# Kernel optimization log

Hardware: AMD Instinct MI355X
Metric: run time of the kernel (lower is better)

The kernel has to match this reference:

```python
import jax, jax.numpy as jnp
import numpy as np

N_NODES = 100000
N_EDGES = 1600000
D = 64


def setup_inputs() -> dict:
    key = jax.random.key(0)
    k1, k2, k3, k4 = jax.random.split(key, 4)
    graph_embedding = jax.random.normal(k1, (N_NODES, D), dtype=jnp.float32)
    # xavier_uniform_ on a (1, D) tensor: bound = sqrt(6 / (1 + D))
    bound = float(np.sqrt(6.0 / (1 + D)))
    weight = jax.random.uniform(k2, (1, D), dtype=jnp.float32, minval=-bound, maxval=bound)
    src = jax.random.randint(k3, (N_EDGES,), 0, N_NODES, dtype=jnp.int32)
    dst = jax.random.randint(k4, (N_EDGES,), 0, N_NODES, dtype=jnp.int32)
    return {"graph_embedding": graph_embedding, "weight": weight, "src": src, "dst": dst}


def reference(graph_embedding, weight, src, dst):
    # emb = elu(x * w) per node, then copy_u/sum over edges:
    # out[d] = sum over edges (s -> d) of emb[s]
    emb = jax.nn.elu(graph_embedding * weight)          # [N, D]
    msgs = emb[src]                                     # [E, D] gathered source messages
    out = jax.ops.segment_sum(msgs, dst, num_segments=graph_embedding.shape[0])
    return out
```

## Files before the change

kernel.cpp:

```cpp
#include <hip/hip_runtime.h>

#define D 64
#define D4 (D / 4)
#define SBSHIFT 9
#define SBROWS 512
#define CHUNK_E 8192
#define STAGE_CAP 8704
#define NCH_MAX 256
#define NSB_MAX 256

typedef float f32x4 __attribute__((ext_vector_type(4)));

__device__ __forceinline__ float elu1(float z) {
    return z > 0.0f ? z : expm1f(z);
}

__device__ __forceinline__ unsigned int bfpair(float a, float b) {
    unsigned int ua = __float_as_uint(a);
    unsigned int ub = __float_as_uint(b);
    ua = (ua + 0x7FFFu + ((ua >> 16) & 1u)) >> 16;
    ub = (ub + 0x7FFFu + ((ub >> 16) & 1u)) & 0xFFFF0000u;
    return ub | ua;
}

__device__ __forceinline__ float bl16(int u) {
    return __uint_as_float((unsigned)u << 16);
}
__device__ __forceinline__ float bh16(int u) {
    return __uint_as_float((unsigned)u & 0xFFFF0000u);
}

__global__ __launch_bounds__(512) void chunk_emb_kernel(
        const float* __restrict__ x, const float* __restrict__ w,
        uint4* __restrict__ emb16,
        const int* __restrict__ src, const int* __restrict__ dst,
        int* __restrict__ slots_lin,
        int* __restrict__ cbase,
        int total8, int n_edges) {
    __shared__ int hist[256], base[256], cur[256];
    __shared__ int wsum[4];
    __shared__ int stage[CHUNK_E];
    const int tid = threadIdx.x;
    const int lane = tid & 63, wid = tid >> 6;

    if (tid < 256) hist[tid] = 0;
    const int gsz = gridDim.x * 512;
    for (int i = blockIdx.x * 512 + tid; i < total8; i += gsz) {
        f32x4 a = __builtin_nontemporal_load((const f32x4*)x + 2 * i);
        f32x4 b = __builtin_nontemporal_load((const f32x4*)x + 2 * i + 1);
        float4 wa = ((const float4*)w)[(2 * i) & 15];
        float4 wb = ((const float4*)w)[(2 * i + 1) & 15];
        uint4 o;
        o.x = bfpair(elu1(a.x * wa.x), elu1(a.y * wa.y));
        o.y = bfpair(elu1(a.z * wa.z), elu1(a.w * wa.w));
        o.z = bfpair(elu1(b.x * wb.x), elu1(b.y * wb.y));
        o.w = bfpair(elu1(b.z * wb.z), elu1(b.w * wb.w));
        emb16[i] = o;
    }

    const int c0  = blockIdx.x * CHUNK_E;
    const int kn  = min(CHUNK_E, n_edges - c0);
    const int kn4 = kn >> 2;
    const int tail = kn & 3;
    __syncthreads();
    const int4* dst4 = (const int4*)(dst + c0);
    for (int k = tid; k < kn4; k += 512) {
        int4 dv = dst4[k];
        atomicAdd(&hist[dv.x >> SBSHIFT], 1);
        atomicAdd(&hist[dv.y >> SBSHIFT], 1);
        atomicAdd(&hist[dv.z >> SBSHIFT], 1);
        atomicAdd(&hist[dv.w >> SBSHIFT], 1);
    }
    if (tid < tail)
        atomicAdd(&hist[dst[c0 + (kn4 << 2) + tid] >> SBSHIFT], 1);
    __syncthreads();
    int h = 0, incl = 0;
    if (tid < 256) {
        h = hist[tid];
        incl = h;
        #pragma unroll
        for (int off = 1; off < 64; off <<= 1) {
            int t = __shfl_up(incl, off, 64);
            if (lane >= off) incl += t;
        }
        if (lane == 63) wsum[wid] = incl;
    }
    __syncthreads();
    if (tid < 256) {
        int pre = 0;
        for (int k = 0; k < wid; k++) pre += wsum[k];
        int e = pre + incl - h;
        base[tid] = e;
        cur[tid]  = e;
    }
    __syncthreads();
    const int4* src4 = (const int4*)(src + c0);
    for (int k = tid; k < kn4; k += 512) {
        int4 dv = dst4[k];
        int4 sv = src4[k];
        int pos;
        pos = atomicAdd(&cur[dv.x >> SBSHIFT], 1);
        stage[pos] = ((dv.x & (SBROWS - 1)) << 17) | sv.x;
        pos = atomicAdd(&cur[dv.y >> SBSHIFT], 1);
        stage[pos] = ((dv.y & (SBROWS - 1)) << 17) | sv.y;
        pos = atomicAdd(&cur[dv.z >> SBSHIFT], 1);
        stage[pos] = ((dv.z & (SBROWS - 1)) << 17) | sv.z;
        pos = atomicAdd(&cur[dv.w >> SBSHIFT], 1);
        stage[pos] = ((dv.w & (SBROWS - 1)) << 17) | sv.w;
    }
    if (tid < tail) {
        int k = (kn4 << 2) + tid;
        int d = dst[c0 + k], s = src[c0 + k];
        int pos = atomicAdd(&cur[d >> SBSHIFT], 1);
        stage[pos] = ((d & (SBROWS - 1)) << 17) | s;
    }
    __syncthreads();
    for (int j = tid; j < kn; j += 512)
        slots_lin[c0 + j] = stage[j];
    if (tid < 256) cbase[blockIdx.x * 257 + tid] = base[tid];
    if (tid == 0)  cbase[blockIdx.x * 257 + 256] = kn;
}

__global__ __launch_bounds__(512) void fine_sort_kernel(
        const int* __restrict__ slots_lin,
        const int* __restrict__ cbase,
        int* __restrict__ sorted2,
        int* __restrict__ node_off,
        int n_nodes, int NCH) {
    __shared__ int rstart[NCH_MAX], rc[NCH_MAX];
    __shared__ int counts[SBROWS], cur[SBROWS];
    __shared__ int wsum[8], swa[8], swt[8];
    __shared__ int stage_out[STAGE_CAP];
    const int s = blockIdx.x;
    const int tid = threadIdx.x;
    const int wid = tid >> 6, lane = tid & 63;
    const int sg = tid >> 4, l16 = tid & 15;

    int va = 0, vt = 0;
    if (tid < NCH) {
        int a = cbase[tid * 257 + s];
        int b = cbase[tid * 257 + s + 1];
        rstart[tid] = tid * CHUNK_E + a;
        rc[tid] = b - a;
        va = a;
        vt = b - a;
    }
    #pragma unroll
    for (int off = 1; off < 64; off <<= 1) {
        va += __shfl_xor(va, off, 64);
        vt += __shfl_xor(vt, off, 64);
    }
    if (lane == 0) { swa[wid] = va; swt[wid] = vt; }
    counts[tid] = 0;
    __syncthreads();
    int sbb = 0, T = 0;
    #pragma unroll
    for (int k = 0; k < 8; k++) { sbb += swa[k]; T += swt[k]; }
    const bool fast = (T <= STAGE_CAP);
    for (int c = sg; c < NCH; c += 32) {
        int n = rc[c], st = rstart[c];
        for (int j = l16; j < n; j += 16)
            atomicAdd(&counts[((unsigned)slots_lin[st + j]) >> 17], 1);
    }
    __syncthreads();
    int v = counts[tid];
    int incl = v;
    #pragma unroll
    for (int off = 1; off < 64; off <<= 1) {
        int t = __shfl_up(incl, off, 64);
        if (lane >= off) incl += t;
    }
    if (lane == 63) wsum[wid] = incl;
    __syncthreads();
    int pre = 0;
    for (int k = 0; k < wid; k++) pre += wsum[k];
    int e0 = pre + incl - v;
    cur[tid] = fast ? e0 : sbb + e0;
    int g0 = (s << SBSHIFT) + tid;
    if (g0 < n_nodes) node_off[g0] = sbb + e0;
    if (s == gridDim.x - 1 && tid == 0) node_off[n_nodes] = sbb + T;
    __syncthreads();
    for (int c = sg; c < NCH; c += 32) {
        int n = rc[c], st = rstart[c];
        for (int j = l16; j < n; j += 16) {
            int pl = slots_lin[st + j];
            int r = ((unsigned)pl) >> 17;
            int pos = atomicAdd(&cur[r], 1);
            if (fast) stage_out[pos] = pl & 0x1FFFF;
            else      sorted2[pos]   = pl & 0x1FFFF;
        }
    }
    __syncthreads();
    if (fast) {
        for (int i = tid; i < T; i += 512)
            sorted2[sbb + i] = stage_out[i];
    }
}

__global__ void gather_sum_kernel(const unsigned int* __restrict__ emb16,
                                  const int* __restrict__ sorted2,
                                  const int* __restrict__ node_off,
                                  float* __restrict__ out, int n_nodes) {
    int wave = (blockIdx.x * blockDim.x + threadIdx.x) >> 6;
    if (wave >= n_nodes) return;
    const int lane = threadIdx.x & 63;
    const int g = lane >> 3;
    const int c = lane & 7;
    const int beg = node_off[wave], end = node_off[wave + 1];
    const int deg = end - beg;
    const int dmain = min(deg, 64);
    const int4* row = (const int4*)emb16;

    int myidx = 0;
    if (lane < dmain) myidx = __builtin_nontemporal_load(sorted2 + beg + lane);

    float acc[8] = {0.f, 0.f, 0.f, 0.f, 0.f, 0.f, 0.f, 0.f};

    for (int base = 0; base < dmain; base += 32) {
        const int m = dmain - base;
        int s0 = __shfl(myidx, base + g, 64);
        int s1 = __shfl(myidx, base + g + 8, 64);
        int s2 = __shfl(myidx, base + g + 16, 64);
        int s3 = __shfl(myidx, base + g + 24, 64);
        int4 u0 = make_int4(0, 0, 0, 0);
        int4 u1 = make_int4(0, 0, 0, 0);
        int4 u2 = make_int4(0, 0, 0, 0);
        int4 u3 = make_int4(0, 0, 0, 0);
        if (g < m)      u0 = row[s0 * 8 + c];
        if (g + 8 < m)  u1 = row[s1 * 8 + c];
        if (g + 16 < m) u2 = row[s2 * 8 + c];
        if (g + 24 < m) u3 = row[s3 * 8 + c];
        acc[0] += bl16(u0.x) + bl16(u1.x) + bl16(u2.x) + bl16(u3.x);
        acc[1] += bh16(u0.x) + bh16(u1.x) + bh16(u2.x) + bh16(u3.x);
        acc[2] += bl16(u0.y) + bl16(u1.y) + bl16(u2.y) + bl16(u3.y);
        acc[3] += bh16(u0.y) + bh16(u1.y) + bh16(u2.y) + bh16(u3.y);
        acc[4] += bl16(u0.z) + bl16(u1.z) + bl16(u2.z) + bl16(u3.z);
        acc[5] += bh16(u0.z) + bh16(u1.z) + bh16(u2.z) + bh16(u3.z);
        acc[6] += bl16(u0.w) + bl16(u1.w) + bl16(u2.w) + bl16(u3.w);
        acc[7] += bh16(u0.w) + bh16(u1.w) + bh16(u2.w) + bh16(u3.w);
    }
    for (int e = beg + 64 + g; e < end; e += 8) {
        int s0 = __builtin_nontemporal_load(sorted2 + e);
        int4 u0 = row[s0 * 8 + c];
        acc[0] += bl16(u0.x); acc[1] += bh16(u0.x);
        acc[2] += bl16(u0.y); acc[3] += bh16(u0.y);
        acc[4] += bl16(u0.z); acc[5] += bh16(u0.z);
        acc[6] += bl16(u0.w); acc[7] += bh16(u0.w);
    }
    #pragma unroll
    for (int off = 8; off <= 32; off <<= 1) {
        #pragma unroll
        for (int k = 0; k < 8; k++) acc[k] += __shfl_xor(acc[k], off, 64);
    }
    if (g == 0) {
        f32x4* out4 = (f32x4*)out;
        f32x4 o0 = {acc[0], acc[1], acc[2], acc[3]};
        f32x4 o1 = {acc[4], acc[5], acc[6], acc[7]};
        __builtin_nontemporal_store(o0, out4 + wave * D4 + c * 2);
        __builtin_nontemporal_store(o1, out4 + wave * D4 + c * 2 + 1);
    }
}

__global__ void zero_out_kernel(float* __restrict__ out, int total4) {
    int i = blockIdx.x * blockDim.x + threadIdx.x;
    if (i < total4) ((float4*)out)[i] = make_float4(0.f, 0.f, 0.f, 0.f);
}

__global__ void scatter_fused_kernel(const float* __restrict__ x,
                                     const float* __restrict__ w,
                                     const int* __restrict__ src,
                                     const int* __restrict__ dst,
                                     float* __restrict__ out, int n_edges) {
    int t = blockIdx.x * blockDim.x + threadIdx.x;
    int e = t >> 4;
    int c = t & 15;
    if (e >= n_edges) return;
    int s = src[e];
    int d = dst[e];
    float4 xv = ((const float4*)x)[s * D4 + c];
    float4 wv = ((const float4*)w)[c];
    float* o = out + d * D + c * 4;
    unsafeAtomicAdd(o + 0, elu1(xv.x * wv.x));
    unsafeAtomicAdd(o + 1, elu1(xv.y * wv.y));
    unsafeAtomicAdd(o + 2, elu1(xv.z * wv.z));
    unsafeAtomicAdd(o + 3, elu1(xv.w * wv.w));
}

extern "C" void kernel_launch(void* const* d_in, const int* in_sizes, int n_in,
                              void* d_out, int out_size, void* d_ws, size_t ws_size,
                              hipStream_t stream) {
    const float* x   = (const float*)d_in[0];
    const float* w   = (const float*)d_in[1];
    const int*   src = (const int*)d_in[2];
    const int*   dst = (const int*)d_in[3];
    float* out = (float*)d_out;

    const int n_nodes = in_sizes[0] / D;
    const int n_edges = in_sizes[2];
    const int total4  = n_nodes * D4;
    const int total8  = n_nodes * 8;
    const int block = 256;

    const int NSB = (n_nodes + SBROWS - 1) >> SBSHIFT;
    const int NCH = (n_edges + CHUNK_E - 1) / CHUNK_E;

    auto align16 = [](size_t v) { return (v + 15) & ~size_t(15); };
    const size_t emb_b      = align16((size_t)n_nodes * D * 2);
    const size_t slots_b    = align16((size_t)NCH * CHUNK_E * 4);
    const size_t cbase_b    = align16((size_t)NCH * 257 * 4);
    const size_t sorted2_b  = align16((size_t)n_edges * 4);
    const size_t nodeoff_b  = align16((size_t)(n_nodes + 1) * 4);
    const size_t need = emb_b + slots_b + cbase_b + sorted2_b + nodeoff_b;

    if (ws_size >= need && n_nodes <= 131072 && NSB <= NSB_MAX && NCH <= NCH_MAX) {
        char* p = (char*)d_ws;
        unsigned int* emb16 = (unsigned int*)p;  p += emb_b;
        int* slots_lin = (int*)p;  p += slots_b;
        int* cbase     = (int*)p;  p += cbase_b;
        int* sorted2   = (int*)p;  p += sorted2_b;
        int* node_off  = (int*)p;

        chunk_emb_kernel<<<NCH, 512, 0, stream>>>(
            x, w, (uint4*)emb16, src, dst, slots_lin, cbase, total8, n_edges);
        fine_sort_kernel<<<NSB, 512, 0, stream>>>(
            slots_lin, cbase, sorted2, node_off, n_nodes, NCH);
        const int wave_blocks = (n_nodes * 64 + block - 1) / block;
        gather_sum_kernel<<<wave_blocks, block, 0, stream>>>(
            emb16, sorted2, node_off, out, n_nodes);
    } else {
        zero_out_kernel<<<(total4 + block - 1) / block, block, 0, stream>>>(out, total4);
        const int nt = n_edges * 16;
        scatter_fused_kernel<<<(nt + block - 1) / block, block, 0, stream>>>(
            x, w, src, dst, out, n_edges);
    }
}
```

Baseline: 149.7 us.

## Gather eight nodes per wavefront and halve sort chunk and superblock sizes

The gather kernel now assigns eight destination nodes to each wavefront, one per 8-lane group, instead of one node per wave. The wave preloads up to 192 neighbour indices into registers, picks them by shuffle, and drops the cross-group reduction. This removes the idle lanes that low-degree nodes (average degree 16) leave in a 64-lane wave. The sort now uses 4096-edge chunks and 256-row superblocks, so there are twice as many blocks per kernel and the histogram arrays are indexed by NSB. The cost is load imbalance inside a wave, since every group loops to the largest degree among its eight nodes.

New measurement: 141.0 us. -5.8%, faster.

```diff
diff --git a/kernel.cpp b/kernel.cpp
--- a/kernel.cpp
+++ b/kernel.cpp
@@ -2,12 +2,12 @@
 
 #define D 64
 #define D4 (D / 4)
-#define SBSHIFT 9
-#define SBROWS 512
-#define CHUNK_E 8192
-#define STAGE_CAP 8704
-#define NCH_MAX 256
-#define NSB_MAX 256
+#define SBSHIFT 8
+#define SBROWS 256
+#define CHUNK_E 4096
+#define STAGE_CAP 4608
+#define NCH_MAX 512
+#define NSB_MAX 512
 
 typedef float f32x4 __attribute__((ext_vector_type(4)));
 
@@ -36,14 +36,14 @@
         const int* __restrict__ src, const int* __restrict__ dst,
         int* __restrict__ slots_lin,
         int* __restrict__ cbase,
-        int total8, int n_edges) {
-    __shared__ int hist[256], base[256], cur[256];
-    __shared__ int wsum[4];
+        int total8, int n_edges, int NSB) {
+    __shared__ int hist[NSB_MAX], base[NSB_MAX], cur[NSB_MAX];
+    __shared__ int wsum[8];
     __shared__ int stage[CHUNK_E];
     const int tid = threadIdx.x;
     const int lane = tid & 63, wid = tid >> 6;
 
-    if (tid < 256) hist[tid] = 0;
+    hist[tid] = 0;
     const int gsz = gridDim.x * 512;
     for (int i = blockIdx.x * 512 + tid; i < total8; i += gsz) {
         f32x4 a = __builtin_nontemporal_load((const f32x4*)x + 2 * i);
@@ -74,19 +74,16 @@
     if (tid < tail)
         atomicAdd(&hist[dst[c0 + (kn4 << 2) + tid] >> SBSHIFT], 1);
     __syncthreads();
-    int h = 0, incl = 0;
-    if (tid < 256) {
-        h = hist[tid];
-        incl = h;
-        #pragma unroll
-        for (int off = 1; off < 64; off <<= 1) {
-            int t = __shfl_up(incl, off, 64);
-            if (lane >= off) incl += t;
-        }
-        if (lane == 63) wsum[wid] = incl;
-    }
-    __syncthreads();
-    if (tid < 256) {
+    int h = hist[tid];
+    int incl = h;
+    #pragma unroll
+    for (int off = 1; off < 64; off <<= 1) {
+        int t = __shfl_up(incl, off, 64);
+        if (lane >= off) incl += t;
+    }
+    if (lane == 63) wsum[wid] = incl;
+    __syncthreads();
+    {
         int pre = 0;
         for (int k = 0; k < wid; k++) pre += wsum[k];
         int e = pre + incl - h;
@@ -117,8 +114,8 @@
     __syncthreads();
     for (int j = tid; j < kn; j += 512)
         slots_lin[c0 + j] = stage[j];
-    if (tid < 256) cbase[blockIdx.x * 257 + tid] = base[tid];
-    if (tid == 0)  cbase[blockIdx.x * 257 + 256] = kn;
+    if (tid < NSB) cbase[blockIdx.x * (NSB + 1) + tid] = base[tid];
+    if (tid == 0)  cbase[blockIdx.x * (NSB + 1) + NSB] = kn;
 }
 
 __global__ __launch_bounds__(512) void fine_sort_kernel(
@@ -126,10 +123,10 @@
         const int* __restrict__ cbase,
         int* __restrict__ sorted2,
         int* __restrict__ node_off,
-        int n_nodes, int NCH) {
+        int n_nodes, int NCH, int NSB) {
     __shared__ int rstart[NCH_MAX], rc[NCH_MAX];
     __shared__ int counts[SBROWS], cur[SBROWS];
-    __shared__ int wsum[8], swa[8], swt[8];
+    __shared__ int wsum[4], swa[8], swt[8];
     __shared__ int stage_out[STAGE_CAP];
     const int s = blockIdx.x;
     const int tid = threadIdx.x;
@@ -138,8 +135,8 @@
 
     int va = 0, vt = 0;
     if (tid < NCH) {
-        int a = cbase[tid * 257 + s];
-        int b = cbase[tid * 257 + s + 1];
+        int a = cbase[tid * (NSB + 1) + s];
+        int b = cbase[tid * (NSB + 1) + s + 1];
         rstart[tid] = tid * CHUNK_E + a;
         rc[tid] = b - a;
         va = a;
@@ -151,7 +148,7 @@
         vt += __shfl_xor(vt, off, 64);
     }
     if (lane == 0) { swa[wid] = va; swt[wid] = vt; }
-    counts[tid] = 0;
+    if (tid < SBROWS) counts[tid] = 0;
     __syncthreads();
     int sbb = 0, T = 0;
     #pragma unroll
@@ -163,21 +160,26 @@
             atomicAdd(&counts[((unsigned)slots_lin[st + j]) >> 17], 1);
     }
     __syncthreads();
-    int v = counts[tid];
-    int incl = v;
-    #pragma unroll
-    for (int off = 1; off < 64; off <<= 1) {
-        int t = __shfl_up(incl, off, 64);
-        if (lane >= off) incl += t;
-    }
-    if (lane == 63) wsum[wid] = incl;
-    __syncthreads();
-    int pre = 0;
-    for (int k = 0; k < wid; k++) pre += wsum[k];
-    int e0 = pre + incl - v;
-    cur[tid] = fast ? e0 : sbb + e0;
-    int g0 = (s << SBSHIFT) + tid;
-    if (g0 < n_nodes) node_off[g0] = sbb + e0;
+    int v = 0, incl = 0;
+    if (tid < SBROWS) {
+        v = counts[tid];
+        incl = v;
+        #pragma unroll
+        for (int off = 1; off < 64; off <<= 1) {
+            int t = __shfl_up(incl, off, 64);
+            if (lane >= off) incl += t;
+        }
+        if (lane == 63) wsum[wid] = incl;
+    }
+    __syncthreads();
+    if (tid < SBROWS) {
+        int pre = 0;
+        for (int k = 0; k < wid; k++) pre += wsum[k];
+        int e0 = pre + incl - v;
+        cur[tid] = fast ? e0 : sbb + e0;
+        int g0 = (s << SBSHIFT) + tid;
+        if (g0 < n_nodes) node_off[g0] = sbb + e0;
+    }
     if (s == gridDim.x - 1 && tid == 0) node_off[n_nodes] = sbb + T;
     __syncthreads();
     for (int c = sg; c < NCH; c += 32) {
@@ -197,39 +199,71 @@
     }
 }
 
+__device__ __forceinline__ int pick_idx(int p, int m0, int m1, int m2,
+                                        const int* __restrict__ s2, int W0) {
+    int a  = __shfl(m0, p & 63, 64);
+    int b  = __shfl(m1, p & 63, 64);
+    int cc = __shfl(m2, p & 63, 64);
+    int r = p < 64 ? a : (p < 128 ? b : cc);
+    if (p >= 192) r = s2[W0 + p];
+    return r;
+}
+
 __global__ void gather_sum_kernel(const unsigned int* __restrict__ emb16,
                                   const int* __restrict__ sorted2,
                                   const int* __restrict__ node_off,
                                   float* __restrict__ out, int n_nodes) {
-    int wave = (blockIdx.x * blockDim.x + threadIdx.x) >> 6;
-    if (wave >= n_nodes) return;
+    const int wv = (blockIdx.x * blockDim.x + threadIdx.x) >> 6;
     const int lane = threadIdx.x & 63;
     const int g = lane >> 3;
     const int c = lane & 7;
-    const int beg = node_off[wave], end = node_off[wave + 1];
-    const int deg = end - beg;
-    const int dmain = min(deg, 64);
+    const int n0 = wv * 8;
+    if (n0 >= n_nodes) return;
+    const int n = n0 + g;
+
+    int beg = 0, end = 0;
+    if (n < n_nodes) {
+        beg = node_off[n];
+        end = node_off[n + 1];
+    }
+    const int W0   = node_off[n0];
+    const int Wend = node_off[min(n0 + 8, n_nodes)];
+    const int T = Wend - W0;
+
+    int m0 = 0, m1 = 0, m2 = 0;
+    if (lane < T)       m0 = sorted2[W0 + lane];
+    if (64 + lane < T)  m1 = sorted2[W0 + 64 + lane];
+    if (128 + lane < T) m2 = sorted2[W0 + 128 + lane];
+
     const int4* row = (const int4*)emb16;
-
-    int myidx = 0;
-    if (lane < dmain) myidx = __builtin_nontemporal_load(sorted2 + beg + lane);
+    const int pb = beg - W0;
+    const int d = end - beg;
+    int dmax = d;
+    dmax = max(dmax, __shfl_xor(dmax, 8, 64));
+    dmax = max(dmax, __shfl_xor(dmax, 16, 64));
+    dmax = max(dmax, __shfl_xor(dmax, 32, 64));
+    const int pclamp = T - 1;
 
     float acc[8] = {0.f, 0.f, 0.f, 0.f, 0.f, 0.f, 0.f, 0.f};
 
-    for (int base = 0; base < dmain; base += 32) {
-        const int m = dmain - base;
-        int s0 = __shfl(myidx, base + g, 64);
-        int s1 = __shfl(myidx, base + g + 8, 64);
-        int s2 = __shfl(myidx, base + g + 16, 64);
-        int s3 = __shfl(myidx, base + g + 24, 64);
+    int e = 0;
+    for (; e + 4 <= dmax; e += 4) {
+        int p0 = min(max(pb + e,     0), pclamp);
+        int p1 = min(max(pb + e + 1, 0), pclamp);
+        int p2 = min(max(pb + e + 2, 0), pclamp);
+        int p3 = min(max(pb + e + 3, 0), pclamp);
+        int i0 = pick_idx(p0, m0, m1, m2, sorted2, W0);
+        int i1 = pick_idx(p1, m0, m1, m2, sorted2, W0);
+        int i2 = pick_idx(p2, m0, m1, m2, sorted2, W0);
+        int i3 = pick_idx(p3, m0, m1, m2, sorted2, W0);
         int4 u0 = make_int4(0, 0, 0, 0);
         int4 u1 = make_int4(0, 0, 0, 0);
         int4 u2 = make_int4(0, 0, 0, 0);
         int4 u3 = make_int4(0, 0, 0, 0);
-        if (g < m)      u0 = row[s0 * 8 + c];
-        if (g + 8 < m)  u1 = row[s1 * 8 + c];
-        if (g + 16 < m) u2 = row[s2 * 8 + c];
-        if (g + 24 < m) u3 = row[s3 * 8 + c];
+        if (e < d)     u0 = row[i0 * 8 + c];
+        if (e + 1 < d) u1 = row[i1 * 8 + c];
+        if (e + 2 < d) u2 = row[i2 * 8 + c];
+        if (e + 3 < d) u3 = row[i3 * 8 + c];
         acc[0] += bl16(u0.x) + bl16(u1.x) + bl16(u2.x) + bl16(u3.x);
         acc[1] += bh16(u0.x) + bh16(u1.x) + bh16(u2.x) + bh16(u3.x);
         acc[2] += bl16(u0.y) + bl16(u1.y) + bl16(u2.y) + bl16(u3.y);
@@ -239,25 +273,24 @@
         acc[6] += bl16(u0.w) + bl16(u1.w) + bl16(u2.w) + bl16(u3.w);
         acc[7] += bh16(u0.w) + bh16(u1.w) + bh16(u2.w) + bh16(u3.w);
     }
-    for (int e = beg + 64 + g; e < end; e += 8) {
-        int s0 = __builtin_nontemporal_load(sorted2 + e);
-        int4 u0 = row[s0 * 8 + c];
-        acc[0] += bl16(u0.x); acc[1] += bh16(u0.x);
-        acc[2] += bl16(u0.y); acc[3] += bh16(u0.y);
-        acc[4] += bl16(u0.z); acc[5] += bh16(u0.z);
-        acc[6] += bl16(u0.w); acc[7] += bh16(u0.w);
-    }
-    #pragma unroll
-    for (int off = 8; off <= 32; off <<= 1) {
-        #pragma unroll
-        for (int k = 0; k < 8; k++) acc[k] += __shfl_xor(acc[k], off, 64);
-    }
-    if (g == 0) {
+    for (; e < dmax; ++e) {
+        int p0 = min(max(pb + e, 0), pclamp);
+        int i0 = pick_idx(p0, m0, m1, m2, sorted2, W0);
+        if (e < d) {
+            int4 u0 = row[i0 * 8 + c];
+            acc[0] += bl16(u0.x); acc[1] += bh16(u0.x);
+            acc[2] += bl16(u0.y); acc[3] += bh16(u0.y);
+            acc[4] += bl16(u0.z); acc[5] += bh16(u0.z);
+            acc[6] += bl16(u0.w); acc[7] += bh16(u0.w);
+        }
+    }
+
+    if (n < n_nodes) {
         f32x4* out4 = (f32x4*)out;
         f32x4 o0 = {acc[0], acc[1], acc[2], acc[3]};
         f32x4 o1 = {acc[4], acc[5], acc[6], acc[7]};
-        __builtin_nontemporal_store(o0, out4 + wave * D4 + c * 2);
-        __builtin_nontemporal_store(o1, out4 + wave * D4 + c * 2 + 1);
+        __builtin_nontemporal_store(o0, out4 + (size_t)n * D4 + c * 2);
+        __builtin_nontemporal_store(o1, out4 + (size_t)n * D4 + c * 2 + 1);
     }
 }
 
@@ -307,7 +340,7 @@
     auto align16 = [](size_t v) { return (v + 15) & ~size_t(15); };
     const size_t emb_b      = align16((size_t)n_nodes * D * 2);
     const size_t slots_b    = align16((size_t)NCH * CHUNK_E * 4);
-    const size_t cbase_b    = align16((size_t)NCH * 257 * 4);
+    const size_t cbase_b    = align16((size_t)NCH * (NSB + 1) * 4);
     const size_t sorted2_b  = align16((size_t)n_edges * 4);
     const size_t nodeoff_b  = align16((size_t)(n_nodes + 1) * 4);
     const size_t need = emb_b + slots_b + cbase_b + sorted2_b + nodeoff_b;
@@ -321,11 +354,13 @@
         int* node_off  = (int*)p;
 
         chunk_emb_kernel<<<NCH, 512, 0, stream>>>(
-            x, w, (uint4*)emb16, src, dst, slots_lin, cbase, total8, n_edges);
+            x, w, (uint4*)emb16, src, dst, slots_lin, cbase,
+            total8, n_edges, NSB);
         fine_sort_kernel<<<NSB, 512, 0, stream>>>(
-            slots_lin, cbase, sorted2, node_off, n_nodes, NCH);
-        const int wave_blocks = (n_nodes * 64 + block - 1) / block;
-        gather_sum_kernel<<<wave_blocks, block, 0, stream>>>(
+            slots_lin, cbase, sorted2, node_off, n_nodes, NCH, NSB);
+        const int nwaves = (n_nodes + 7) / 8;
+        const int gblocks = (nwaves * 64 + block - 1) / block;
+        gather_sum_kernel<<<gblocks, block, 0, stream>>>(
             emb16, sorted2, node_off, out, n_nodes);
     } else {
         zero_out_kernel<<<(total4 + block - 1) / block, block, 0, stream>>>(out, total4);
```
